# Optimization experiments

Hardware: AMD Instinct MI355X
Metric: run time of the kernel (lower is better)

The kernel has to match this reference:

```python
import jax, jax.numpy as jnp
import numpy as np

H = 4096        # nodes per color (bipartite 2-coloring)
N = 2 * H       # total nodes
D = 8           # true degree
PAD = 2         # -1 padding columns
MD = D + PAD    # max_degree incl. padding
C = 2048        # num_chains
NE = H * D      # number of edges


def _build_graph():
    # color0 node i connects to color1 node H + (i+k)%H, edge index i*D+k
    i = np.arange(H)[:, None]
    k = np.arange(D)[None, :]
    adj0 = H + (i + k) % H            # neighbours of color0 nodes
    w0 = i * D + k                    # flat edge index
    adj1 = (i - k) % H                # neighbours of color1 nodes (inverse map)
    w1 = ((i - k) % H) * D + k
    adj = np.concatenate([adj0, adj1], axis=0)   # [N, D]
    w = np.concatenate([w0, w1], axis=0)
    pad = -np.ones((N, PAD), dtype=np.int64)     # ragged-padding sentinel
    adj = np.concatenate([adj, pad], axis=1)     # [N, MD]
    w = np.concatenate([w, pad], axis=1)
    return jnp.asarray(adj, jnp.int64), jnp.asarray(w, jnp.int64)


def setup_inputs() -> dict:
    key = jax.random.key(0)
    k1, k2, k3 = jax.random.split(key, 3)
    # random +/-1 spins (rands in the torch code)
    x = jnp.where(jax.random.normal(k1, (C, N)) >= 0, 1.0, -1.0).astype(jnp.float32)
    linear = 0.1 * jax.random.normal(k2, (N,), dtype=jnp.float32)
    quadratic = jax.random.normal(k3, (NE,), dtype=jnp.float32) / np.sqrt(D)
    adj, adj_w = _build_graph()
    schedule = jnp.array([0.5, 1.0, 2.0], dtype=jnp.float32)
    block0 = jnp.arange(H, dtype=jnp.int64)
    block1 = jnp.arange(H, N, dtype=jnp.int64)
    return {"x": x, "linear": linear, "quadratic": quadratic,
            "schedule": schedule, "adj": adj, "adj_w": adj_w,
            "block0": block0, "block1": block1}


def reference(x, linear, quadratic, schedule, adj, adj_w, block0, block1):
    """Block-Gibbs spin sampling over an inverse-temperature schedule.

    Faithful to BlockSpinSampler.sample with Gibbs acceptance:
      field = sum_nbr J * x_nbr + h  (padded -1 indices read a zeros column)
      P(spin=+1) = sigmoid(-2*beta*field);  spins in {-1,+1}.
    """
    chains = x.shape[0]
    zeros = jnp.zeros((chains, 1), dtype=x.dtype)
    key = jax.random.key(42)
    blocks = (block0, block1)
    n_steps = schedule.shape[0]  # static
    for t in range(n_steps):
        beta = schedule[t]
        for b, block in enumerate(blocks):
            xz = jnp.concatenate([x, zeros], axis=1)          # [C, N+1]; index -1 -> 0
            xnbr = xz[:, adj[block]]                          # [C, B, MD] padded gather
            Jb = quadratic[adj_w[block]]                      # [B, MD] (pad masked by xnbr==0)
            field = jnp.einsum('cbd,bd->cb', xnbr, Jb) + linear[block]  # [C, B]
            prob = jax.nn.sigmoid(-2.0 * beta * field)        # = 1/(1+exp(2*beta*field))
            sub = jax.random.fold_in(key, t * len(blocks) + b)
            u = jax.random.uniform(sub, prob.shape, dtype=prob.dtype)
            spins = jnp.where(u < prob, 1.0, -1.0).astype(x.dtype)  # bit2spin_soft(bernoulli)
            x = x.at[:, block].set(spins)
    return x
```

## Files before the change

kernel.cpp:

```cpp
#include <hip/hip_runtime.h>
#include <stdint.h>


#define HH 4096
#define NN 8192
#define NCHAIN 2048

__device__ __forceinline__ uint32_t rotl32(uint32_t v, int r) {
  return (v << r) | (v >> (32 - r));
}

__device__ __forceinline__ void tf2x32(uint32_t k0, uint32_t k1,
                                       uint32_t x0, uint32_t x1,
                                       uint32_t& o0, uint32_t& o1) {
  const uint32_t ks2 = k0 ^ k1 ^ 0x1BD11BDAu;
  x0 += k0; x1 += k1;
  x0 += x1; x1 = rotl32(x1, 13); x1 ^= x0;
  x0 += x1; x1 = rotl32(x1, 15); x1 ^= x0;
  x0 += x1; x1 = rotl32(x1, 26); x1 ^= x0;
  x0 += x1; x1 = rotl32(x1, 6);  x1 ^= x0;
  x0 += k1; x1 += ks2 + 1u;
  x0 += x1; x1 = rotl32(x1, 17); x1 ^= x0;
  x0 += x1; x1 = rotl32(x1, 29); x1 ^= x0;
  x0 += x1; x1 = rotl32(x1, 16); x1 ^= x0;
  x0 += x1; x1 = rotl32(x1, 24); x1 ^= x0;
  x0 += ks2; x1 += k0 + 2u;
  x0 += x1; x1 = rotl32(x1, 13); x1 ^= x0;
  x0 += x1; x1 = rotl32(x1, 15); x1 ^= x0;
  x0 += x1; x1 = rotl32(x1, 26); x1 ^= x0;
  x0 += x1; x1 = rotl32(x1, 6);  x1 ^= x0;
  x0 += k0; x1 += k1 + 3u;
  x0 += x1; x1 = rotl32(x1, 17); x1 ^= x0;
  x0 += x1; x1 = rotl32(x1, 29); x1 ^= x0;
  x0 += x1; x1 = rotl32(x1, 16); x1 ^= x0;
  x0 += x1; x1 = rotl32(x1, 24); x1 ^= x0;
  x0 += k1; x1 += ks2 + 4u;
  x0 += x1; x1 = rotl32(x1, 13); x1 ^= x0;
  x0 += x1; x1 = rotl32(x1, 15); x1 ^= x0;
  x0 += x1; x1 = rotl32(x1, 26); x1 ^= x0;
  x0 += x1; x1 = rotl32(x1, 6);  x1 ^= x0;
  o0 = x0 + ks2;
  o1 = x1 + k0 + 5u;
}

__device__ __forceinline__ float xla_expf_nc(float xin) {
#pragma clang fp contract(off)
#define MA(a, b, c) ((a) * (b) + (c))
  float x = xin;
  float fx = floorf(MA(x, 1.44269504088896341f, 0.5f));
  float tmp = 0.693359375f * fx;
  float z = -2.12194440e-4f * fx;
  x = x - tmp;
  x = x - z;
  z = x * x;
  float y = MA(x, 1.9875691500e-4f, 1.3981999507e-3f);
  y = MA(y, x, 8.3334519073e-3f);
  y = MA(y, x, 4.1665795894e-2f);
  y = MA(y, x, 1.6666665459e-1f);
  y = MA(y, x, 5.0000001201e-1f);
  y = MA(y, z, x);
  y = y + 1.0f;
  int n = (int)fx;
  float two_n = __int_as_float((uint32_t)(n + 127) << 23);
  return y * two_n;
#undef MA
}

__device__ __forceinline__ float recip1(float d) {
  const float q0 = __builtin_amdgcn_rcpf(d);
  const float e0 = __builtin_fmaf(-d, q0, 1.0f);
  return __builtin_fmaf(q0, e0, q0);
}

__global__ __launch_bounds__(256) void prep_kernel(
    const float* __restrict__ quad, float* __restrict__ qt,
    uint32_t* __restrict__ keys) {
  int idx = blockIdx.x * 256 + threadIdx.x;
  if (idx < 8 * HH) {
    int h = idx >> 3, k = idx & 7;
    qt[idx] = quad[(((h - k) & (HH - 1)) << 3) + k];
  }
  if (blockIdx.x == 0 && threadIdx.x < 6) {
    uint32_t a, b;
    tf2x32(0u, 42u, 0u, (uint32_t)threadIdx.x, a, b);
    keys[2 * threadIdx.x] = a;
    keys[2 * threadIdx.x + 1] = b;
  }
}

template <int B>
__device__ __forceinline__ void half_step(int tid, uint32_t cbase, float* row,
                                          const float* __restrict__ qw,
                                          const float* __restrict__ lin,
                                          float scale, uint32_t sk0,
                                          uint32_t sk1) {
  const float* rd = (B == 0) ? (row + HH) : row;
  float* wr = (B == 0) ? row : (row + HH);
  for (int j = 0; j < 16; ++j) {
    const int h = tid + j * 256;
    const float* qbase = qw + 8 * h;
    const float4 qa = *(const float4*)qbase;
    const float4 qb = *(const float4*)(qbase + 4);

    float acc = 0.0f;
    if (B == 0) {
      if (h <= HH - 8) {
        const float* p = rd + h;
        acc = __builtin_fmaf(p[0], qa.x, acc);
        acc = __builtin_fmaf(p[1], qa.y, acc);
        acc = __builtin_fmaf(p[2], qa.z, acc);
        acc = __builtin_fmaf(p[3], qa.w, acc);
        acc = __builtin_fmaf(p[4], qb.x, acc);
        acc = __builtin_fmaf(p[5], qb.y, acc);
        acc = __builtin_fmaf(p[6], qb.z, acc);
        acc = __builtin_fmaf(p[7], qb.w, acc);
      } else {
        const float qs[8] = {qa.x, qa.y, qa.z, qa.w, qb.x, qb.y, qb.z, qb.w};
#pragma unroll
        for (int k = 0; k < 8; ++k)
          acc = __builtin_fmaf(rd[(h + k) & (HH - 1)], qs[k], acc);
      }
    } else {
      if (h >= 7) {
        const float* p = rd + h - 7;
        acc = __builtin_fmaf(p[7], qa.x, acc);
        acc = __builtin_fmaf(p[6], qa.y, acc);
        acc = __builtin_fmaf(p[5], qa.z, acc);
        acc = __builtin_fmaf(p[4], qa.w, acc);
        acc = __builtin_fmaf(p[3], qb.x, acc);
        acc = __builtin_fmaf(p[2], qb.y, acc);
        acc = __builtin_fmaf(p[1], qb.z, acc);
        acc = __builtin_fmaf(p[0], qb.w, acc);
      } else {
        const float qs[8] = {qa.x, qa.y, qa.z, qa.w, qb.x, qb.y, qb.z, qb.w};
#pragma unroll
        for (int k = 0; k < 8; ++k)
          acc = __builtin_fmaf(rd[(h - k) & (HH - 1)], qs[k], acc);
      }
    }
    const float field = acc + lin[h];

    const float e = xla_expf_nc(scale * field);
    const float prob = recip1(1.0f + e);

    uint32_t b0, b1;
    tf2x32(sk0, sk1, 0u, cbase + (uint32_t)(j * 256), b0, b1);
    const uint32_t bits = b0 ^ b1;
    const float u = __uint_as_float((bits >> 9) | 0x3f800000u) - 1.0f;

    wr[h] = (u < prob) ? 1.0f : -1.0f;
  }
}

template <bool USE_QT>
__global__ __launch_bounds__(256) void gibbs_kernel(
    const float* __restrict__ x_in, const float* __restrict__ linear,
    const float* __restrict__ quad, const float* __restrict__ qt,
    const float* __restrict__ sched, const uint32_t* __restrict__ keys,
    float* __restrict__ x_out) {
  __shared__ float row[NN];
  const int c = blockIdx.x;
  const int tid = threadIdx.x;
  const uint32_t cbase = (uint32_t)c * HH + (uint32_t)tid;

  {
    const float4* src = (const float4*)(x_in + (size_t)c * NN);
    float4* dst = (float4*)row;
    for (int j = tid; j < NN / 4; j += 256) dst[j] = src[j];
  }
  __syncthreads();

#pragma unroll
  for (int t = 0; t < 3; ++t) {
    const float scale = 2.0f * sched[t];
    uint32_t k00, k01, k10, k11;
    if (USE_QT) {
      k00 = keys[4 * t + 0]; k01 = keys[4 * t + 1];
      k10 = keys[4 * t + 2]; k11 = keys[4 * t + 3];
    } else {
      tf2x32(0u, 42u, 0u, (uint32_t)(2 * t), k00, k01);
      tf2x32(0u, 42u, 0u, (uint32_t)(2 * t + 1), k10, k11);
    }
    half_step<0>(tid, cbase, row, quad, linear, scale, k00, k01);
    __syncthreads();
    if (USE_QT) {
      half_step<1>(tid, cbase, row, qt, linear + HH, scale, k10, k11);
    } else {
      for (int j = 0; j < 16; ++j) {
        const int h = tid + j * 256;
        float acc = 0.0f;
#pragma unroll
        for (int k = 0; k < 8; ++k) {
          const int nb = (h - k) & (HH - 1);
          acc = __builtin_fmaf(row[nb], quad[8 * nb + k], acc);
        }
        const float field = acc + linear[HH + h];
        const float e = xla_expf_nc(scale * field);
        const float prob = recip1(1.0f + e);
        uint32_t b0, b1;
        tf2x32(k10, k11, 0u, cbase + (uint32_t)(j * 256), b0, b1);
        const float u =
            __uint_as_float(((b0 ^ b1) >> 9) | 0x3f800000u) - 1.0f;
        row[HH + h] = (u < prob) ? 1.0f : -1.0f;
      }
    }
    __syncthreads();
  }

  {
    const float4* src = (const float4*)row;
    float4* dst = (float4*)(x_out + (size_t)c * NN);
    for (int j = tid; j < NN / 4; j += 256) dst[j] = src[j];
  }
}

extern "C" void kernel_launch(void* const* d_in, const int* in_sizes, int n_in,
                              void* d_out, int out_size, void* d_ws,
                              size_t ws_size, hipStream_t stream) {
  const float* x = (const float*)d_in[0];
  const float* linear = (const float*)d_in[1];
  const float* quad = (const float*)d_in[2];
  const float* sched = (const float*)d_in[3];
  float* out = (float*)d_out;

  const size_t need = (size_t)(8 * HH) * sizeof(float) + 16 * sizeof(uint32_t);
  if (ws_size >= need) {
    float* qt = (float*)d_ws;
    uint32_t* keys =
        (uint32_t*)((char*)d_ws + (size_t)(8 * HH) * sizeof(float));
    hipLaunchKernelGGL(prep_kernel, dim3((8 * HH + 255) / 256), dim3(256), 0,
                       stream, quad, qt, keys);
    hipLaunchKernelGGL((gibbs_kernel<true>), dim3(NCHAIN), dim3(256), 0,
                       stream, x, linear, quad, qt, sched, keys, out);
  } else {
    hipLaunchKernelGGL((gibbs_kernel<false>), dim3(NCHAIN), dim3(256), 0,
                       stream, x, linear, quad, (const float*)nullptr, sched,
                       (const uint32_t*)nullptr, out);
  }
}
```

Baseline: 181.7 us.

## Use hardware exp2/rcp fast path with exact fallback near decision boundary

Each thread now handles two nodes per iteration. The probability is computed with a hardware exp2 and rcp, and the bit-exact polynomial exp plus Newton reciprocal only runs when some lane's uniform sample falls within a small relative bracket around the fast probability. The exact path is also packed into two-wide vector ops to allow packed FP32 instructions. This cuts transcendental ALU work in the common case, at the cost of wave-level divergence checks and the risk that the bracket is too narrow to guarantee identical spins.

```diff
diff --git a/kernel.cpp b/kernel.cpp
--- a/kernel.cpp
+++ b/kernel.cpp
@@ -5,6 +5,8 @@
 #define HH 4096
 #define NN 8192
 #define NCHAIN 2048
+
+typedef float v2f __attribute__((ext_vector_type(2)));
 
 __device__ __forceinline__ uint32_t rotl32(uint32_t v, int r) {
   return (v << r) | (v >> (32 - r));
@@ -43,33 +45,47 @@
   o1 = x1 + k0 + 5u;
 }
 
-__device__ __forceinline__ float xla_expf_nc(float xin) {
+__device__ __forceinline__ float exp2_hw(float x) {
+#if __has_builtin(__builtin_amdgcn_exp2f)
+  return __builtin_amdgcn_exp2f(x);
+#else
+  float r;
+  asm("v_exp_f32 %0, %1" : "=v"(r) : "v"(x));
+  return r;
+#endif
+}
+
+__device__ __forceinline__ v2f xla_expf_pk(v2f xin) {
 #pragma clang fp contract(off)
-#define MA(a, b, c) ((a) * (b) + (c))
-  float x = xin;
-  float fx = floorf(MA(x, 1.44269504088896341f, 0.5f));
-  float tmp = 0.693359375f * fx;
-  float z = -2.12194440e-4f * fx;
+  v2f x = xin;
+  v2f fx = __builtin_elementwise_floor(x * 1.44269504088896341f + 0.5f);
+  v2f tmp = fx * 0.693359375f;
+  v2f z = fx * -2.12194440e-4f;
   x = x - tmp;
   x = x - z;
   z = x * x;
-  float y = MA(x, 1.9875691500e-4f, 1.3981999507e-3f);
-  y = MA(y, x, 8.3334519073e-3f);
-  y = MA(y, x, 4.1665795894e-2f);
-  y = MA(y, x, 1.6666665459e-1f);
-  y = MA(y, x, 5.0000001201e-1f);
-  y = MA(y, z, x);
+  v2f y = x * 1.9875691500e-4f + 1.3981999507e-3f;
+  y = y * x + 8.3334519073e-3f;
+  y = y * x + 4.1665795894e-2f;
+  y = y * x + 1.6666665459e-1f;
+  y = y * x + 5.0000001201e-1f;
+  y = y * z + x;
   y = y + 1.0f;
-  int n = (int)fx;
-  float two_n = __int_as_float((uint32_t)(n + 127) << 23);
+  const int na = (int)fx.x;
+  const int nb = (int)fx.y;
+  v2f two_n;
+  two_n.x = __int_as_float((uint32_t)(na << 23) + 0x3f800000u);
+  two_n.y = __int_as_float((uint32_t)(nb << 23) + 0x3f800000u);
   return y * two_n;
-#undef MA
-}
-
-__device__ __forceinline__ float recip1(float d) {
-  const float q0 = __builtin_amdgcn_rcpf(d);
-  const float e0 = __builtin_fmaf(-d, q0, 1.0f);
-  return __builtin_fmaf(q0, e0, q0);
+}
+
+__device__ __forceinline__ v2f recip_pk(v2f d) {
+  v2f q0;
+  q0.x = __builtin_amdgcn_rcpf(d.x);
+  q0.y = __builtin_amdgcn_rcpf(d.y);
+  const v2f one2 = {1.0f, 1.0f};
+  v2f e0 = __builtin_elementwise_fma(-d, q0, one2);
+  return __builtin_elementwise_fma(q0, e0, q0);
 }
 
 __global__ __launch_bounds__(256) void prep_kernel(
@@ -87,6 +103,52 @@
     keys[2 * threadIdx.x + 1] = b;
   }
 }
+
+template <int B>
+__device__ __forceinline__ float dot8(const float* __restrict__ rd,
+                                      const float* __restrict__ qw, int h) {
+  const float4 qa = *(const float4*)(qw + 8 * h);
+  const float4 qb = *(const float4*)(qw + 8 * h + 4);
+  float acc = 0.0f;
+  if (B == 0) {
+    if (h <= HH - 8) {
+      const float* p = rd + h;
+      acc = __builtin_fmaf(p[0], qa.x, acc);
+      acc = __builtin_fmaf(p[1], qa.y, acc);
+      acc = __builtin_fmaf(p[2], qa.z, acc);
+      acc = __builtin_fmaf(p[3], qa.w, acc);
+      acc = __builtin_fmaf(p[4], qb.x, acc);
+      acc = __builtin_fmaf(p[5], qb.y, acc);
+      acc = __builtin_fmaf(p[6], qb.z, acc);
+      acc = __builtin_fmaf(p[7], qb.w, acc);
+    } else {
+      const float qs[8] = {qa.x, qa.y, qa.z, qa.w, qb.x, qb.y, qb.z, qb.w};
+#pragma unroll
+      for (int k = 0; k < 8; ++k)
+        acc = __builtin_fmaf(rd[(h + k) & (HH - 1)], qs[k], acc);
+    }
+  } else {
+    if (h >= 7) {
+      const float* p = rd + h - 7;
+      acc = __builtin_fmaf(p[7], qa.x, acc);
+      acc = __builtin_fmaf(p[6], qa.y, acc);
+      acc = __builtin_fmaf(p[5], qa.z, acc);
+      acc = __builtin_fmaf(p[4], qa.w, acc);
+      acc = __builtin_fmaf(p[3], qb.x, acc);
+      acc = __builtin_fmaf(p[2], qb.y, acc);
+      acc = __builtin_fmaf(p[1], qb.z, acc);
+      acc = __builtin_fmaf(p[0], qb.w, acc);
+    } else {
+      const float qs[8] = {qa.x, qa.y, qa.z, qa.w, qb.x, qb.y, qb.z, qb.w};
+#pragma unroll
+      for (int k = 0; k < 8; ++k)
+        acc = __builtin_fmaf(rd[(h - k) & (HH - 1)], qs[k], acc);
+    }
+  }
+  return acc;
+}
+
+#define EPS_BRACKET 6.103515625e-05f
 
 template <int B>
 __device__ __forceinline__ void half_step(int tid, uint32_t cbase, float* row,
@@ -96,59 +158,39 @@
                                           uint32_t sk1) {
   const float* rd = (B == 0) ? (row + HH) : row;
   float* wr = (B == 0) ? row : (row + HH);
-  for (int j = 0; j < 16; ++j) {
-    const int h = tid + j * 256;
-    const float* qbase = qw + 8 * h;
-    const float4 qa = *(const float4*)qbase;
-    const float4 qb = *(const float4*)(qbase + 4);
-
-    float acc = 0.0f;
-    if (B == 0) {
-      if (h <= HH - 8) {
-        const float* p = rd + h;
-        acc = __builtin_fmaf(p[0], qa.x, acc);
-        acc = __builtin_fmaf(p[1], qa.y, acc);
-        acc = __builtin_fmaf(p[2], qa.z, acc);
-        acc = __builtin_fmaf(p[3], qa.w, acc);
-        acc = __builtin_fmaf(p[4], qb.x, acc);
-        acc = __builtin_fmaf(p[5], qb.y, acc);
-        acc = __builtin_fmaf(p[6], qb.z, acc);
-        acc = __builtin_fmaf(p[7], qb.w, acc);
-      } else {
-        const float qs[8] = {qa.x, qa.y, qa.z, qa.w, qb.x, qb.y, qb.z, qb.w};
-#pragma unroll
-        for (int k = 0; k < 8; ++k)
-          acc = __builtin_fmaf(rd[(h + k) & (HH - 1)], qs[k], acc);
-      }
-    } else {
-      if (h >= 7) {
-        const float* p = rd + h - 7;
-        acc = __builtin_fmaf(p[7], qa.x, acc);
-        acc = __builtin_fmaf(p[6], qa.y, acc);
-        acc = __builtin_fmaf(p[5], qa.z, acc);
-        acc = __builtin_fmaf(p[4], qa.w, acc);
-        acc = __builtin_fmaf(p[3], qb.x, acc);
-        acc = __builtin_fmaf(p[2], qb.y, acc);
-        acc = __builtin_fmaf(p[1], qb.z, acc);
-        acc = __builtin_fmaf(p[0], qb.w, acc);
-      } else {
-        const float qs[8] = {qa.x, qa.y, qa.z, qa.w, qb.x, qb.y, qb.z, qb.w};
-#pragma unroll
-        for (int k = 0; k < 8; ++k)
-          acc = __builtin_fmaf(rd[(h - k) & (HH - 1)], qs[k], acc);
-      }
-    }
-    const float field = acc + lin[h];
-
-    const float e = xla_expf_nc(scale * field);
-    const float prob = recip1(1.0f + e);
-
-    uint32_t b0, b1;
-    tf2x32(sk0, sk1, 0u, cbase + (uint32_t)(j * 256), b0, b1);
-    const uint32_t bits = b0 ^ b1;
-    const float u = __uint_as_float((bits >> 9) | 0x3f800000u) - 1.0f;
-
-    wr[h] = (u < prob) ? 1.0f : -1.0f;
+  for (int jj = 0; jj < 8; ++jj) {
+    const int ha = tid + jj * 512;
+    const int hb = ha + 256;
+    v2f acc2 = {dot8<B>(rd, qw, ha), dot8<B>(rd, qw, hb)};
+    v2f lin2 = {lin[ha], lin[hb]};
+    v2f field = acc2 + lin2;
+    v2f xin = field * scale;
+
+    v2f ef = {exp2_hw(xin.x * 1.4426950408889634f),
+              exp2_hw(xin.y * 1.4426950408889634f)};
+    v2f d = ef + 1.0f;
+    v2f pf = {__builtin_amdgcn_rcpf(d.x), __builtin_amdgcn_rcpf(d.y)};
+    v2f lo = pf * (1.0f - EPS_BRACKET);
+    v2f hi = pf * (1.0f + EPS_BRACKET);
+
+    uint32_t a0, a1, b0, b1;
+    const uint32_t ia = cbase + (uint32_t)(jj * 512);
+    tf2x32(sk0, sk1, 0u, ia, a0, a1);
+    tf2x32(sk0, sk1, 0u, ia + 256u, b0, b1);
+    v2f u;
+    u.x = __uint_as_float(((a0 ^ a1) >> 9) | 0x3f800000u);
+    u.y = __uint_as_float(((b0 ^ b1) >> 9) | 0x3f800000u);
+    u = u - 1.0f;
+
+    v2f p_use = pf;
+    const bool bl = (u.x >= lo.x && u.x < hi.x) ||
+                    (u.y >= lo.y && u.y < hi.y);
+    if (__any(bl)) {
+      v2f e_ex = xla_expf_pk(xin);
+      p_use = recip_pk(e_ex + 1.0f);
+    }
+    wr[ha] = (u.x < p_use.x) ? 1.0f : -1.0f;
+    wr[hb] = (u.y < p_use.y) ? 1.0f : -1.0f;
   }
 }
 
@@ -195,13 +237,14 @@
           acc = __builtin_fmaf(row[nb], quad[8 * nb + k], acc);
         }
         const float field = acc + linear[HH + h];
-        const float e = xla_expf_nc(scale * field);
-        const float prob = recip1(1.0f + e);
+        v2f xin2 = {scale * field, scale * field};
+        v2f e2 = xla_expf_pk(xin2);
+        v2f p2 = recip_pk(e2 + 1.0f);
         uint32_t b0, b1;
         tf2x32(k10, k11, 0u, cbase + (uint32_t)(j * 256), b0, b1);
         const float u =
             __uint_as_float(((b0 ^ b1) >> 9) | 0x3f800000u) - 1.0f;
-        row[HH + h] = (u < prob) ? 1.0f : -1.0f;
+        row[HH + h] = (u < p2.x) ? 1.0f : -1.0f;
       }
     }
     __syncthreads();
```

Result: faster. 174.6 us (-3.9%).
